# Kernel tuning notes

Measured on AMD Instinct MI355X. Metric: run time of the kernel, lower is better.

Reference implementation:

```python
import jax, jax.numpy as jnp
import numpy as np

NUM_HEADS = 16


def setup_inputs() -> dict:
    key = jax.random.key(0)
    ks = jax.random.split(key, 6)
    dim = 1024
    B, N = 4, 4096
    s = 1.0 / np.sqrt(dim)
    return {
        "x": jax.random.normal(ks[0], (B, N, dim), dtype=jnp.float32),
        "Wq": jax.random.normal(ks[1], (dim, dim), dtype=jnp.float32) * s,
        "Wk": jax.random.normal(ks[2], (dim, dim), dtype=jnp.float32) * s,
        "Wv": jax.random.normal(ks[3], (dim, dim), dtype=jnp.float32) * s,
        "Wo": jax.random.normal(ks[4], (dim, dim), dtype=jnp.float32) * s,
        "bo": jnp.zeros((dim,), dtype=jnp.float32),
    }


def reference(x, Wq, Wk, Wv, Wo, bo):
    # STAtten (linear attention) branch, no SNN, dropout = 0 (identity in eval).
    B, N, C = x.shape
    H = NUM_HEADS
    D = C // H
    scale = D ** (-0.5)

    def heads(W):
        # torch nn.Linear: y = x @ W.T ; then [B,N,H,D] -> [B,H,N,D]
        y = jnp.einsum('bnc,oc->bno', x, W)
        return y.reshape(B, N, H, D).transpose(0, 2, 1, 3)

    q = heads(Wq)
    k = heads(Wk)
    v = heads(Wv)

    kv = jnp.einsum('bhnd,bhne->bhde', k, v) * scale  # [B,H,D,D]
    out = jnp.einsum('bhnd,bhde->bhne', q, kv)        # [B,H,N,D]

    out = out.transpose(0, 2, 1, 3).reshape(B, N, C)
    return jnp.einsum('bnc,oc->bno', out, Wo) + bo
```

## Files before the change

### kernel.cpp

```cpp
#include <hip/hip_runtime.h>
#include <hip/hip_bf16.h>
#include <math.h>

typedef __hip_bfloat16 bf16;
typedef float f32x4 __attribute__((ext_vector_type(4)));
typedef short s16x8 __attribute__((ext_vector_type(8)));

typedef const __attribute__((address_space(1))) void* as1cvp;
typedef __attribute__((address_space(3))) void* as3vp;

__device__ __forceinline__ unsigned short f2bf(float f) {
  unsigned u = __float_as_uint(f);
  u += 0x7FFFu + ((u >> 16) & 1u);
  return (unsigned short)(u >> 16);
}
__device__ __forceinline__ float bf2f(unsigned short s) {
  return __uint_as_float(((unsigned)s) << 16);
}

__device__ __forceinline__ void gpu_barrier() {
  asm volatile("" ::: "memory");
  __builtin_amdgcn_s_barrier();
  asm volatile("" ::: "memory");
}

__device__ __forceinline__ void tri_decode(int xt, int* ti_out, int* tj_out) {
  int tj = (int)((sqrtf(8.0f * (float)xt + 1.0f) - 1.0f) * 0.5f);
  int tri = tj * (tj + 1) / 2;
  if (xt < tri) { --tj; tri = tj * (tj + 1) / 2; }
  else if (xt >= tri + tj + 1) { ++tj; tri = tj * (tj + 1) / 2; }
  *ti_out = xt - tri;
  *tj_out = tj;
}

__global__ __launch_bounds__(256) void cast_transpose(const float* __restrict__ x,
                                                      unsigned short* __restrict__ xb,
                                                      unsigned short* __restrict__ xT) {
  __shared__ unsigned short tl[128 * 136];
  const int n0 = blockIdx.x * 128, d0 = blockIdx.y * 128, b = blockIdx.z;
  const int t = threadIdx.x;

  const int rr0 = t >> 4;
  const int u   = t & 15;
  const int dd  = u * 8;
#pragma unroll
  for (int it = 0; it < 8; ++it) {
    const int rr = rr0 + it * 16;
    const float* src = x + ((long)(b * 4096 + n0 + rr)) * 1024 + d0 + dd;
    f32x4 v0 = *(const f32x4*)src;
    f32x4 v1 = *(const f32x4*)(src + 4);
    s16x8 o;
    o[0] = (short)f2bf(v0[0]); o[1] = (short)f2bf(v0[1]);
    o[2] = (short)f2bf(v0[2]); o[3] = (short)f2bf(v0[3]);
    o[4] = (short)f2bf(v1[0]); o[5] = (short)f2bf(v1[1]);
    o[6] = (short)f2bf(v1[2]); o[7] = (short)f2bf(v1[3]);
    *(s16x8*)&xb[((long)(b * 4096 + n0 + rr)) * 1024 + d0 + dd] = o;
    const int phys = u ^ (rr >> 3);
    *(s16x8*)&tl[rr * 136 + phys * 8] = o;
  }
  __syncthreads();

  const int nblk = t & 15, dblk = t >> 4;
  s16x8 row[8];
#pragma unroll
  for (int j = 0; j < 8; ++j) {
    const int n = nblk * 8 + j;
    const int phys = dblk ^ nblk;
    row[j] = *(const s16x8*)&tl[n * 136 + phys * 8];
  }
#pragma unroll
  for (int c = 0; c < 8; ++c) {
    s16x8 col;
#pragma unroll
    for (int j = 0; j < 8; ++j) col[j] = row[j][c];
    *(s16x8*)&xT[((long)(b * 1024 + d0 + dblk * 8 + c)) * 4096 + n0 + nblk * 8] = col;
  }
}

__global__ __launch_bounds__(256) void cast_weights(const float* __restrict__ Wq,
                                                    const float* __restrict__ Wk,
                                                    const float* __restrict__ Wv,
                                                    const float* __restrict__ Wo,
                                                    unsigned short* __restrict__ Wkb,
                                                    unsigned short* __restrict__ WvD,
                                                    unsigned short* __restrict__ Wqb,
                                                    unsigned short* __restrict__ Wob) {
  const int i = blockIdx.x * 256 + threadIdx.x;
  const int seg = blockIdx.y;
  const long flat = (long)i * 8;
  const float* src = (seg == 0) ? Wk : (seg == 1) ? Wv : (seg == 2) ? Wq : Wo;
  f32x4 v0 = *(const f32x4*)&src[flat];
  f32x4 v1 = *(const f32x4*)&src[flat + 4];
  s16x8 o;
  o[0] = (short)f2bf(v0[0]); o[1] = (short)f2bf(v0[1]);
  o[2] = (short)f2bf(v0[2]); o[3] = (short)f2bf(v0[3]);
  o[4] = (short)f2bf(v1[0]); o[5] = (short)f2bf(v1[1]);
  o[6] = (short)f2bf(v1[2]); o[7] = (short)f2bf(v1[3]);
  if (seg == 1) {
    const int r = (int)(flat >> 10), c = (int)(flat & 1023);
    *(s16x8*)&WvD[(long)r * 2048 + c] = o;
    *(s16x8*)&WvD[(long)r * 2048 + c + 1024] = o;
  } else {
    unsigned short* dst = (seg == 0) ? Wkb : (seg == 2) ? Wqb : Wob;
    *(s16x8*)&dst[flat] = o;
  }
}

template<bool OUTF32>
__global__ __launch_bounds__(512, 2) void gemm256(
    const bf16* __restrict__ A, int lda, long aOffY, long aOffZ,
    const bf16* __restrict__ Bt, int ldb, long btOffY, long btOffZ,
    void* __restrict__ Cv, int ldc, long cOffY, long cOffZ,
    const float* __restrict__ bias, int K, int NtN, int gridmode)
{
  __shared__ char lds[131072];

  const int Nx = gridDim.x, Ny = gridDim.y;
  const int lin = blockIdx.x + Nx * (blockIdx.y + Ny * blockIdx.z);
  const int tot = Nx * Ny * gridDim.z;
  const int swz = (lin & 7) * (tot >> 3) + (lin >> 3);
  const int xt = swz % Nx;
  const int r2 = swz / Nx;
  const int y = r2 % Ny, z = r2 / Ny;
  int ti, tj;
  if (gridmode == 1) {
    ti = (int)((0x3221110000ULL >> (4 * xt)) & 15);
    tj = (int)((0x3323213210ULL >> (4 * xt)) & 15);
  } else { ti = xt / NtN; tj = xt % NtN; }
  const int bm = ti * 256, bn = tj * 256;

  A  += (long)z * aOffZ + (long)y * aOffY;
  Bt += (long)z * btOffZ + (long)y * btOffY;

  const int tid  = threadIdx.x;
  const int wid  = tid >> 6;
  const int lane = tid & 63;
  const int wm = wid >> 2;
  const int wn = wid & 3;
  const int frow = lane & 15;
  const int fkb  = (lane >> 4) << 4;
  const unsigned xorv = (unsigned)((lane & 7) << 4);

  const int q0 = (tid * 16) ^ (((tid >> 3) & 7) << 4);
  const int q1 = (8192 + tid * 16) ^ (((tid >> 3) & 7) << 4);
  const int srow0 = q0 >> 7, scol0 = (q0 & 127) >> 1;
  const int srow1 = q1 >> 7, scol1 = (q1 & 127) >> 1;
  const bf16* ag0 = A  + (long)(bm + srow0) * lda + scol0;
  const bf16* ag1 = A  + (long)(bm + srow1) * lda + scol1;
  const bf16* bg0 = Bt + (long)(bn + srow0) * ldb + scol0;
  const bf16* bg1 = Bt + (long)(bn + srow1) * ldb + scol1;

#define STAGE_A(buf, half, kk) do {                                                  \
    __builtin_amdgcn_global_load_lds((as1cvp)(ag0 + (long)(half)*128*lda + (kk)),    \
        (as3vp)(lds + (buf)*32768 + (half)*16384 + wid*1024), 16, 0, 0);             \
    __builtin_amdgcn_global_load_lds((as1cvp)(ag1 + (long)(half)*128*lda + (kk)),    \
        (as3vp)(lds + (buf)*32768 + (half)*16384 + 8192 + wid*1024), 16, 0, 0);      \
  } while (0)
#define STAGE_B(buf, half, kk) do {                                                  \
    __builtin_amdgcn_global_load_lds((as1cvp)(bg0 + (long)(half)*128*ldb + (kk)),    \
        (as3vp)(lds + 65536 + (buf)*32768 + (half)*16384 + wid*1024), 16, 0, 0);     \
    __builtin_amdgcn_global_load_lds((as1cvp)(bg1 + (long)(half)*128*ldb + (kk)),    \
        (as3vp)(lds + 65536 + (buf)*32768 + (half)*16384 + 8192 + wid*1024), 16, 0, 0); \
  } while (0)

  const unsigned paBase = (unsigned)((wm * 64 + frow) * 128 + fkb);
  const unsigned pbBase = (unsigned)(((wn & 1) * 64 + frow) * 128 + fkb);
  const unsigned bHalf  = (unsigned)((wn >> 1) * 16384);

#define RD_A(dst, cur, Mh, mi, kh)                                                   \
  dst = *(const s16x8*)(lds + (cur)*32768 + (Mh)*16384 +                             \
                        ((paBase + (mi)*2048u + (kh)*64u) ^ xorv))
#define RD_B(dst, cur, nj, kh)                                                       \
  dst = *(const s16x8*)(lds + 65536 + (cur)*32768 + bHalf +                          \
                        ((pbBase + (nj)*2048u + (kh)*64u) ^ xorv))

#define MFMA16(base, bb)                                                             \
  __builtin_amdgcn_s_setprio(1);                                                     \
  _Pragma("unroll")                                                                  \
  for (int mi = 0; mi < 4; ++mi)                                                     \
    _Pragma("unroll")                                                                \
    for (int nj = 0; nj < 4; ++nj)                                                   \
      acc[(base) + mi][nj] = __builtin_amdgcn_mfma_f32_16x16x32_bf16(                \
          a[mi], bb[nj], acc[(base) + mi][nj], 0, 0, 0);                             \
  __builtin_amdgcn_s_setprio(0);

#define LGKM0 asm volatile("s_waitcnt lgkmcnt(0)" ::: "memory")
#define VM8   asm volatile("s_waitcnt vmcnt(8)" ::: "memory")

  f32x4 acc[8][4] = {};
  s16x8 a[4], b0[4], b1[4];
  const int NT = K >> 6;

  STAGE_A(0, 0, 0); STAGE_B(0, 0, 0); STAGE_B(0, 1, 0);
  STAGE_A(0, 1, 0);
  {
    const int kk = (NT > 1) ? 64 : 0;
    STAGE_A(1, 0, kk); STAGE_B(1, 0, kk); STAGE_B(1, 1, kk);
  }
  VM8;
  gpu_barrier();

  for (int t = 0; t < NT; ++t) {
    const int cur = t & 1, nxt = cur ^ 1;
    const int k1 = ((t + 1 < NT) ? (t + 1) : 0) * 64;
    const int k2 = ((t + 2 < NT) ? (t + 2) : 0) * 64;

#pragma unroll
    for (int mi = 0; mi < 4; ++mi) RD_A(a[mi], cur, 0, mi, 0);
#pragma unroll
    for (int nj = 0; nj < 4; ++nj) RD_B(b0[nj], cur, nj, 0);
    STAGE_A(nxt, 1, k1);
    gpu_barrier(); LGKM0;
    MFMA16(0, b0)
    gpu_barrier();

#pragma unroll
    for (int mi = 0; mi < 4; ++mi) RD_A(a[mi], cur, 0, mi, 1);
#pragma unroll
    for (int nj = 0; nj < 4; ++nj) RD_B(b1[nj], cur, nj, 1);
    gpu_barrier(); LGKM0;
    MFMA16(0, b1)
    VM8;
    gpu_barrier();

#pragma unroll
    for (int mi = 0; mi < 4; ++mi) RD_A(a[mi], cur, 1, mi, 0);
    STAGE_A(cur, 0, k2); STAGE_B(cur, 0, k2); STAGE_B(cur, 1, k2);
    gpu_barrier(); LGKM0;
    MFMA16(4, b0)
    gpu_barrier();

#pragma unroll
    for (int mi = 0; mi < 4; ++mi) RD_A(a[mi], cur, 1, mi, 1);
    gpu_barrier(); LGKM0;
    MFMA16(4, b1)
    VM8;
    gpu_barrier();
  }

  asm volatile("s_waitcnt vmcnt(0)" ::: "memory");

  const int crow0 = bm + wm * 64 + (lane >> 4) * 4;
  const int ccol0 = bn + wn * 64 + (lane & 15);
  if (OUTF32) {
    float* C = (float*)Cv + (long)z * cOffZ + (long)y * cOffY;
    float bs[4];
#pragma unroll
    for (int j = 0; j < 4; ++j) bs[j] = bias ? bias[ccol0 + j * 16] : 0.0f;
#pragma unroll
    for (int i = 0; i < 8; ++i) {
      const int row = crow0 + (i >> 2) * 128 + (i & 3) * 16;
#pragma unroll
      for (int j = 0; j < 4; ++j) {
        const int col = ccol0 + j * 16;
#pragma unroll
        for (int r = 0; r < 4; ++r)
          C[(long)(row + r) * ldc + col] = acc[i][j][r] + bs[j];
      }
    }
  } else {
    unsigned short* C = (unsigned short*)Cv + (long)z * cOffZ + (long)y * cOffY;
#pragma unroll
    for (int i = 0; i < 8; ++i) {
      const int row = crow0 + (i >> 2) * 128 + (i & 3) * 16;
#pragma unroll
      for (int j = 0; j < 4; ++j) {
        const int col = ccol0 + j * 16;
#pragma unroll
        for (int r = 0; r < 4; ++r)
          C[(long)(row + r) * ldc + col] = f2bf(acc[i][j][r]);
      }
    }
  }
#undef STAGE_A
#undef STAGE_B
#undef RD_A
#undef RD_B
#undef MFMA16
#undef LGKM0
#undef VM8
}

template<int MODE>
__global__ __launch_bounds__(256) void gemm128(
    const bf16* __restrict__ A0, const bf16* __restrict__ B0,
    void* __restrict__ Cv, const float* __restrict__ bias)
{
  __shared__ char lds[65536];

  const int Nx = gridDim.x;
  const int lin = blockIdx.x + Nx * blockIdx.y;
  const int tot = Nx * gridDim.y;
  const int swz = (lin & 7) * (tot >> 3) + (lin >> 3);
  const int xt = swz % Nx, yy = swz / Nx;

  const int lda = (MODE == 0) ? 4096 : 1024;
  const int ldb = lda;
  const int K   = 1024;
  int bm, bn;
  const bf16 *A, *Bt;
  if (MODE == 0) {
    int ti, tj; tri_decode(xt, &ti, &tj);
    bm = ti * 128; bn = tj * 128;
    const int z = yy >> 2, ys = yy & 3;
    A  = A0 + (long)z * 4194304 + ys * 1024;
    Bt = A;
  } else {
    bm = (xt >> 3) * 128; bn = (xt & 7) * 128;
    A  = A0;
    Bt = B0 + (long)yy * 1048576L;
  }

  const int tid  = threadIdx.x;
  const int wid  = tid >> 6;
  const int lane = tid & 63;
  const int wr = (wid >> 1) * 64, wc = (wid & 1) * 64;
  const int frow = lane & 15;
  const int fkb  = (lane >> 4) << 4;
  const unsigned xorv = (unsigned)((lane & 7) << 4);

  const int q0 = (tid * 16) ^ (((tid >> 3) & 7) << 4);
  const int srow0 = q0 >> 7, scol0 = (q0 & 127) >> 1;
  const bf16* ag = A  + (long)(bm + srow0) * lda + scol0;
  const bf16* bg = Bt + (long)(bn + srow0) * ldb + scol0;

#define STG128(buf, kk) do {                                                         \
    _Pragma("unroll")                                                                \
    for (int i = 0; i < 4; ++i) {                                                    \
      __builtin_amdgcn_global_load_lds((as1cvp)(ag + (long)i * 32 * lda + (kk)),     \
          (as3vp)(lds + (buf) * 16384 + i * 4096 + tid * 16), 16, 0, 0);             \
      __builtin_amdgcn_global_load_lds((as1cvp)(bg + (long)i * 32 * ldb + (kk)),     \
          (as3vp)(lds + 32768 + (buf) * 16384 + i * 4096 + tid * 16), 16, 0, 0);     \
    }                                                                                \
  } while (0)

  const unsigned paB = (unsigned)((wr + frow) * 128 + fkb);
  const unsigned pbB = (unsigned)((wc + frow) * 128 + fkb);

  f32x4 acc[4][4] = {};
  const int NT = K >> 6;

  STG128(0, 0);
  asm volatile("s_waitcnt vmcnt(0)" ::: "memory");
  gpu_barrier();

  for (int t = 0; t < NT; ++t) {
    const int cur = t & 1;
    if (t + 1 < NT) STG128(cur ^ 1, (t + 1) * 64);
    s16x8 a[4][2], b[4][2];
#pragma unroll
    for (int mi = 0; mi < 4; ++mi)
#pragma unroll
      for (int kh = 0; kh < 2; ++kh)
        a[mi][kh] = *(const s16x8*)(lds + cur * 16384 +
                                    ((paB + mi * 2048u + kh * 64u) ^ xorv));
#pragma unroll
    for (int nj = 0; nj < 4; ++nj)
#pragma unroll
      for (int kh = 0; kh < 2; ++kh)
        b[nj][kh] = *(const s16x8*)(lds + 32768 + cur * 16384 +
                                    ((pbB + nj * 2048u + kh * 64u) ^ xorv));
    asm volatile("s_waitcnt lgkmcnt(0)" ::: "memory");
#pragma unroll
    for (int mi = 0; mi < 4; ++mi)
#pragma unroll
      for (int nj = 0; nj < 4; ++nj) {
        acc[mi][nj] = __builtin_amdgcn_mfma_f32_16x16x32_bf16(a[mi][0], b[nj][0], acc[mi][nj], 0, 0, 0);
        acc[mi][nj] = __builtin_amdgcn_mfma_f32_16x16x32_bf16(a[mi][1], b[nj][1], acc[mi][nj], 0, 0, 0);
      }
    asm volatile("s_waitcnt vmcnt(0)" ::: "memory");
    gpu_barrier();
  }

  const int r0 = wr + (lane >> 4) * 4;
  const int c0t = wc + (lane & 15);
  if (MODE == 0) {
    float* C = (float*)Cv + (long)(yy * 36 + xt) * 16384;
#pragma unroll
    for (int mi = 0; mi < 4; ++mi)
#pragma unroll
      for (int nj = 0; nj < 4; ++nj)
#pragma unroll
        for (int r = 0; r < 4; ++r)
          C[(r0 + mi * 16 + r) * 128 + c0t + nj * 16] = acc[mi][nj][r];
  } else if (MODE == 2) {
    unsigned short* C = (unsigned short*)Cv + (long)yy * 2097152;
#pragma unroll
    for (int mi = 0; mi < 4; ++mi)
#pragma unroll
      for (int nj = 0; nj < 4; ++nj)
#pragma unroll
        for (int r = 0; r < 4; ++r) {
          const float v = acc[mi][nj][r];
          const unsigned short h = f2bf(v);
          const long idx = (long)(bm + r0 + mi * 16 + r) * 2048 + bn + c0t + nj * 16;
          C[idx] = h;
          C[idx + 1024] = f2bf(v - bf2f(h));
        }
  } else {
    unsigned short* C = (unsigned short*)Cv + (long)yy * 1048576;
#pragma unroll
    for (int mi = 0; mi < 4; ++mi)
#pragma unroll
      for (int nj = 0; nj < 4; ++nj)
#pragma unroll
        for (int r = 0; r < 4; ++r)
          C[(long)(bm + r0 + mi * 16 + r) * 1024 + bn + c0t + nj * 16] =
              f2bf(acc[mi][nj][r]);
  }
#undef STG128
}

__global__ __launch_bounds__(256) void gred128(const float* __restrict__ Gp,
                                               unsigned short* __restrict__ Gb) {
  const int tile = blockIdx.x >> 2, sub = blockIdx.x & 3;
  const int z = blockIdx.y;
  int ti, tj; tri_decode(tile, &ti, &tj);
  const int t = threadIdx.x;
  const int rr = sub * 32 + (t >> 3);
  const int c0 = (t & 7) * 16;

  f32x4 s[4] = {};
#pragma unroll
  for (int y = 0; y < 4; ++y) {
    const float* p = Gp + ((long)(z * 4 + y) * 36 + tile) * 16384 + rr * 128 + c0;
#pragma unroll
    for (int q = 0; q < 4; ++q) {
      f32x4 v = *(const f32x4*)&p[q * 4];
#pragma unroll
      for (int j = 0; j < 4; ++j) s[q][j] += v[j];
    }
  }
  unsigned short hi[16];
#pragma unroll
  for (int q = 0; q < 4; ++q)
#pragma unroll
    for (int j = 0; j < 4; ++j) hi[q * 4 + j] = f2bf(s[q][j]);
  unsigned short* base = Gb + (long)z * 1048576;
  const int R0 = ti * 128 + rr, C0 = tj * 128 + c0;
#pragma unroll
  for (int q = 0; q < 2; ++q)
    *(s16x8*)&base[(long)R0 * 1024 + C0 + q * 8] = *(const s16x8*)&hi[q * 8];
  if (ti != tj) {
#pragma unroll
    for (int j = 0; j < 16; ++j)
      base[(long)(C0 + j) * 1024 + R0] = hi[j];
  }
}

template<int OUTMODE>
__global__ __launch_bounds__(256) void gemm64(
    const bf16* __restrict__ A, int lda, long aOffZ,
    const bf16* __restrict__ Bt, int ldb, long btOffZ,
    void* __restrict__ Cv, int ldc, long cOffZ, int loOff,
    int K, int NtN, int diag, int ksplit)
{
  __shared__ char lds[32768];

  const int Nx = gridDim.x;
  const int lin = blockIdx.x + Nx * blockIdx.y;
  const int tot = Nx * gridDim.y;
  const int swz = (lin & 7) * (tot >> 3) + (lin >> 3);
  const int xt = swz % Nx, y = swz / Nx;
  const int zb = y / ksplit, zs = y % ksplit;
  const int ti = diag ? xt : xt / NtN;
  const int tj = diag ? xt : xt % NtN;
  const int bm = ti * 64, bn = tj * 64;

  A  += (long)zb * aOffZ + (long)zs * K;
  Bt += (long)zb * btOffZ + (long)zs * K;

  const int tid  = threadIdx.x;
  const int wid  = tid >> 6;
  const int lane = tid & 63;
  const int wr = (wid >> 1) * 32, wc = (wid & 1) * 32;
  const int frow = lane & 15;
  const int fkb  = (lane >> 4) << 4;
  const unsigned xorv = (unsigned)((lane & 7) << 4);

  const int q0 = (tid * 16) ^ (((tid >> 3) & 7) << 4);
  const int q1 = (4096 + tid * 16) ^ (((tid >> 3) & 7) << 4);
  const int srow0 = q0 >> 7, scol0 = (q0 & 127) >> 1;
  const int srow1 = q1 >> 7, scol1 = (q1 & 127) >> 1;
  const bf16* ag0 = A  + (long)(bm + srow0) * lda + scol0;
  const bf16* ag1 = A  + (long)(bm + srow1) * lda + scol1;
  const bf16* bg0 = Bt + (long)(bn + srow0) * ldb + scol0;
  const bf16* bg1 = Bt + (long)(bn + srow1) * ldb + scol1;

#define STAGE64(buf, kk) do {                                                        \
    __builtin_amdgcn_global_load_lds((as1cvp)(ag0 + (kk)),                           \
        (as3vp)(lds + (buf)*8192 + wid*1024), 16, 0, 0);                             \
    __builtin_amdgcn_global_load_lds((as1cvp)(ag1 + (kk)),                           \
        (as3vp)(lds + (buf)*8192 + 4096 + wid*1024), 16, 0, 0);                      \
    __builtin_amdgcn_global_load_lds((as1cvp)(bg0 + (kk)),                           \
        (as3vp)(lds + 16384 + (buf)*8192 + wid*1024), 16, 0, 0);                     \
    __builtin_amdgcn_global_load_lds((as1cvp)(bg1 + (kk)),                           \
        (as3vp)(lds + 16384 + (buf)*8192 + 4096 + wid*1024), 16, 0, 0);              \
  } while (0)

  const unsigned paB = (unsigned)((wr + frow) * 128 + fkb);
  const unsigned pbB = (unsigned)((wc + frow) * 128 + fkb);

  f32x4 acc[2][2] = {};
  const int NT = K >> 6;

  STAGE64(0, 0);
  asm volatile("s_waitcnt vmcnt(0)" ::: "memory");
  gpu_barrier();

  for (int t = 0; t < NT; ++t) {
    const int cur = t & 1;
    if (t + 1 < NT) STAGE64(cur ^ 1, (t + 1) * 64);
    s16x8 a[2][2], b[2][2];
#pragma unroll
    for (int mi = 0; mi < 2; ++mi)
#pragma unroll
      for (int kh = 0; kh < 2; ++kh)
        a[mi][kh] = *(const s16x8*)(lds + cur * 8192 +
                                    ((paB + mi * 2048u + kh * 64u) ^ xorv));
#pragma unroll
    for (int nj = 0; nj < 2; ++nj)
#pragma unroll
      for (int kh = 0; kh < 2; ++kh)
        b[nj][kh] = *(const s16x8*)(lds + 16384 + cur * 8192 +
                                    ((pbB + nj * 2048u + kh * 64u) ^ xorv));
    asm volatile("s_waitcnt lgkmcnt(0)" ::: "memory");
#pragma unroll
    for (int mi = 0; mi < 2; ++mi)
#pragma unroll
      for (int nj = 0; nj < 2; ++nj) {
        acc[mi][nj] = __builtin_amdgcn_mfma_f32_16x16x32_bf16(a[mi][0], b[nj][0], acc[mi][nj], 0, 0, 0);
        acc[mi][nj] = __builtin_amdgcn_mfma_f32_16x16x32_bf16(a[mi][1], b[nj][1], acc[mi][nj], 0, 0, 0);
      }
    asm volatile("s_waitcnt vmcnt(0)" ::: "memory");
    gpu_barrier();
  }

  const int r0 = wr + (lane >> 4) * 4;
  const int c0 = wc + (lane & 15);
  if (OUTMODE == 1) {
    float* C = (float*)Cv + (long)y * cOffZ + (long)xt * 4096;
#pragma unroll
    for (int mi = 0; mi < 2; ++mi)
#pragma unroll
      for (int nj = 0; nj < 2; ++nj)
#pragma unroll
        for (int r = 0; r < 4; ++r)
          C[(r0 + mi * 16 + r) * 64 + c0 + nj * 16] = acc[mi][nj][r];
  } else {
    unsigned short* C = (unsigned short*)Cv + (long)y * cOffZ;
#pragma unroll
    for (int mi = 0; mi < 2; ++mi)
#pragma unroll
      for (int nj = 0; nj < 2; ++nj)
#pragma unroll
        for (int r = 0; r < 4; ++r) {
          const float v = acc[mi][nj][r];
          const unsigned short h = f2bf(v);
          const long idx = (long)(bm + r0 + mi * 16 + r) * ldc + bn + c0 + nj * 16;
          C[idx] = h;
          if (OUTMODE == 2) C[idx + loOff] = f2bf(v - bf2f(h));
        }
  }
#undef STAGE64
}

__global__ __launch_bounds__(256) void yt_kernel(const float* __restrict__ Up,
                                                 const unsigned short* __restrict__ Wqb,
                                                 unsigned short* __restrict__ Yt) {
  __shared__ float Ul[64 * 64];
  __shared__ float Wql[64 * 68];
  const int cblk = blockIdx.x, h = blockIdx.y, z = blockIdx.z;
  const int t = threadIdx.x;

  {
    const int d = t >> 2, e0 = (t & 3) * 16;
#pragma unroll
    for (int q = 0; q < 4; ++q) {
      f32x4 s = {};
#pragma unroll
      for (int sp = 0; sp < 4; ++sp) {
        f32x4 v = *(const f32x4*)&Up[((long)(z * 4 + sp) * 16 + h) * 4096 + d * 64 + e0 + q * 4];
#pragma unroll
        for (int j = 0; j < 4; ++j) s[j] += v[j];
      }
      *(f32x4*)&Ul[d * 64 + e0 + q * 4] = s;
    }
    const unsigned short* wp = Wqb + (long)(h * 64 + d) * 1024 + cblk * 64 + e0;
#pragma unroll
    for (int q = 0; q < 2; ++q) {
      s16x8 w = *(const s16x8*)&wp[q * 8];
#pragma unroll
      for (int j = 0; j < 8; ++j) Wql[d * 68 + e0 + q * 8 + j] = bf2f((unsigned short)w[j]);
    }
  }
  __syncthreads();

  const int jc = t >> 2, e0 = (t & 3) * 16;
  f32x4 acc[4] = {};
  for (int d = 0; d < 64; ++d) {
    const float w = Wql[d * 68 + jc];
    const float* ur = &Ul[d * 64 + e0];
#pragma unroll
    for (int q = 0; q < 4; ++q) {
      f32x4 u4 = *(const f32x4*)&ur[q * 4];
#pragma unroll
      for (int j = 0; j < 4; ++j) acc[q][j] += w * u4[j];
    }
  }
  unsigned short* yp = Yt + (long)z * 1048576 + (long)(cblk * 64 + jc) * 1024 + h * 64 + e0;
#pragma unroll
  for (int q = 0; q < 4; ++q)
#pragma unroll
    for (int j = 0; j < 4; ++j) yp[q * 4 + j] = f2bf(acc[q][j] * 0.125f);
}

extern "C" void kernel_launch(void* const* d_in, const int* in_sizes, int n_in,
                              void* d_out, int out_size, void* d_ws, size_t ws_size,
                              hipStream_t stream) {
  const float* x  = (const float*)d_in[0];
  const float* Wq = (const float*)d_in[1];
  const float* Wk = (const float*)d_in[2];
  const float* Wv = (const float*)d_in[3];
  const float* Wo = (const float*)d_in[4];
  const float* bo = (const float*)d_in[5];
  float* out = (float*)d_out;

  char* ws = (char*)d_ws;
  unsigned short* xb  = (unsigned short*)(ws);
  unsigned short* xT  = (unsigned short*)(ws + 33554432);
  unsigned short* Gb  = (unsigned short*)(ws + 33554432);
  unsigned short* Wkb = (unsigned short*)(ws + 67108864);
  unsigned short* WvD = (unsigned short*)(ws + 71303168);
  unsigned short* Wqb = (unsigned short*)(ws + 75497472);
  unsigned short* Wob = (unsigned short*)(ws + 77594624);
  float*          Gp  = (float*)         (ws + 79691776);
  unsigned short* Thl = (unsigned short*)(ws + 79691776);
  float*          Up  = (float*)         (ws + 96468992);
  unsigned short* Yt  = (unsigned short*)(ws + 113246208);
  unsigned short* R   = (unsigned short*)(ws + 121634816);

  cast_transpose<<<dim3(32, 8, 4), 256, 0, stream>>>(x, xb, xT);
  cast_weights<<<dim3(512, 4), 256, 0, stream>>>(Wq, Wk, Wv, Wo, Wkb, WvD, Wqb, Wob);

  gemm128<0><<<dim3(36, 16), 256, 0, stream>>>(
      (const bf16*)xT, nullptr, (void*)Gp, nullptr);

  gred128<<<dim3(144, 4), 256, 0, stream>>>(Gp, Gb);

  gemm128<2><<<dim3(64, 4), 256, 0, stream>>>(
      (const bf16*)Wkb, (const bf16*)Gb, (void*)Thl, nullptr);

  gemm64<1><<<dim3(16, 16), 256, 0, stream>>>(
      (const bf16*)Thl, 2048, 2097152L, (const bf16*)WvD, 2048, 0L,
      (void*)Up, 64, 65536L, 0, 512, 1, 1, 4);

  yt_kernel<<<dim3(16, 16, 4), 256, 0, stream>>>(Up, Wqb, Yt);

  gemm128<3><<<dim3(64, 4), 256, 0, stream>>>(
      (const bf16*)Wob, (const bf16*)Yt, (void*)R, nullptr);

  gemm256<true><<<dim3(64, 1, 4), 512, 0, stream>>>(
      (const bf16*)xb, 1024, 0L, 4194304L,
      (const bf16*)R, 1024, 0L, 1048576L,
      (void*)out, 1024, 0L, 4194304L,
      bo, 1024, 4, 0);
}
```

Measured before the change: 178.9 us.

## Drop hi/lo bf16 split and store Gram partials as bf16

The Gram-matrix partial tiles are now written as bf16 instead of fp32, which halves the traffic for the write and for the reduction read. The hi/lo compensated split of the Wk·G product and the duplicated Wv operand are removed, so the following GEMM runs with half the K (256 instead of 512) and half the operand bytes. The cost is lower precision: partial sums are rounded to bf16 before the reduction, and the error-compensation term is gone, which may push numerical error toward tolerance limits.

```diff
diff --git a/kernel.cpp b/kernel.cpp
--- a/kernel.cpp
+++ b/kernel.cpp
@@ -82,7 +82,7 @@
                                                     const float* __restrict__ Wv,
                                                     const float* __restrict__ Wo,
                                                     unsigned short* __restrict__ Wkb,
-                                                    unsigned short* __restrict__ WvD,
+                                                    unsigned short* __restrict__ Wvb,
                                                     unsigned short* __restrict__ Wqb,
                                                     unsigned short* __restrict__ Wob) {
   const int i = blockIdx.x * 256 + threadIdx.x;
@@ -96,14 +96,8 @@
   o[2] = (short)f2bf(v0[2]); o[3] = (short)f2bf(v0[3]);
   o[4] = (short)f2bf(v1[0]); o[5] = (short)f2bf(v1[1]);
   o[6] = (short)f2bf(v1[2]); o[7] = (short)f2bf(v1[3]);
-  if (seg == 1) {
-    const int r = (int)(flat >> 10), c = (int)(flat & 1023);
-    *(s16x8*)&WvD[(long)r * 2048 + c] = o;
-    *(s16x8*)&WvD[(long)r * 2048 + c + 1024] = o;
-  } else {
-    unsigned short* dst = (seg == 0) ? Wkb : (seg == 2) ? Wqb : Wob;
-    *(s16x8*)&dst[flat] = o;
-  }
+  unsigned short* dst = (seg == 0) ? Wkb : (seg == 1) ? Wvb : (seg == 2) ? Wqb : Wob;
+  *(s16x8*)&dst[flat] = o;
 }
 
 template<bool OUTF32>
@@ -375,28 +369,14 @@
   const int r0 = wr + (lane >> 4) * 4;
   const int c0t = wc + (lane & 15);
   if (MODE == 0) {
-    float* C = (float*)Cv + (long)(yy * 36 + xt) * 16384;
+    unsigned short* C = (unsigned short*)Cv + (long)(yy * 36 + xt) * 16384;
 #pragma unroll
     for (int mi = 0; mi < 4; ++mi)
 #pragma unroll
       for (int nj = 0; nj < 4; ++nj)
 #pragma unroll
         for (int r = 0; r < 4; ++r)
-          C[(r0 + mi * 16 + r) * 128 + c0t + nj * 16] = acc[mi][nj][r];
-  } else if (MODE == 2) {
-    unsigned short* C = (unsigned short*)Cv + (long)yy * 2097152;
-#pragma unroll
-    for (int mi = 0; mi < 4; ++mi)
-#pragma unroll
-      for (int nj = 0; nj < 4; ++nj)
-#pragma unroll
-        for (int r = 0; r < 4; ++r) {
-          const float v = acc[mi][nj][r];
-          const unsigned short h = f2bf(v);
-          const long idx = (long)(bm + r0 + mi * 16 + r) * 2048 + bn + c0t + nj * 16;
-          C[idx] = h;
-          C[idx + 1024] = f2bf(v - bf2f(h));
-        }
+          C[(r0 + mi * 16 + r) * 128 + c0t + nj * 16] = f2bf(acc[mi][nj][r]);
   } else {
     unsigned short* C = (unsigned short*)Cv + (long)yy * 1048576;
 #pragma unroll
@@ -411,7 +391,7 @@
 #undef STG128
 }
 
-__global__ __launch_bounds__(256) void gred128(const float* __restrict__ Gp,
+__global__ __launch_bounds__(256) void gred128(const unsigned short* __restrict__ Gp,
                                                unsigned short* __restrict__ Gb) {
   const int tile = blockIdx.x >> 2, sub = blockIdx.x & 3;
   const int z = blockIdx.y;
@@ -420,22 +400,20 @@
   const int rr = sub * 32 + (t >> 3);
   const int c0 = (t & 7) * 16;
 
-  f32x4 s[4] = {};
+  float s[16] = {};
 #pragma unroll
   for (int y = 0; y < 4; ++y) {
-    const float* p = Gp + ((long)(z * 4 + y) * 36 + tile) * 16384 + rr * 128 + c0;
-#pragma unroll
-    for (int q = 0; q < 4; ++q) {
-      f32x4 v = *(const f32x4*)&p[q * 4];
-#pragma unroll
-      for (int j = 0; j < 4; ++j) s[q][j] += v[j];
+    const unsigned short* p = Gp + ((long)(z * 4 + y) * 36 + tile) * 16384 + rr * 128 + c0;
+#pragma unroll
+    for (int q = 0; q < 2; ++q) {
+      s16x8 v = *(const s16x8*)&p[q * 8];
+#pragma unroll
+      for (int j = 0; j < 8; ++j) s[q * 8 + j] += bf2f((unsigned short)v[j]);
     }
   }
   unsigned short hi[16];
 #pragma unroll
-  for (int q = 0; q < 4; ++q)
-#pragma unroll
-    for (int j = 0; j < 4; ++j) hi[q * 4 + j] = f2bf(s[q][j]);
+  for (int j = 0; j < 16; ++j) hi[j] = f2bf(s[j]);
   unsigned short* base = Gb + (long)z * 1048576;
   const int R0 = ti * 128 + rr, C0 = tj * 128 + c0;
 #pragma unroll
@@ -631,29 +609,29 @@
   unsigned short* xT  = (unsigned short*)(ws + 33554432);
   unsigned short* Gb  = (unsigned short*)(ws + 33554432);
   unsigned short* Wkb = (unsigned short*)(ws + 67108864);
-  unsigned short* WvD = (unsigned short*)(ws + 71303168);
+  unsigned short* Wvb = (unsigned short*)(ws + 71303168);
   unsigned short* Wqb = (unsigned short*)(ws + 75497472);
   unsigned short* Wob = (unsigned short*)(ws + 77594624);
-  float*          Gp  = (float*)         (ws + 79691776);
-  unsigned short* Thl = (unsigned short*)(ws + 79691776);
+  unsigned short* Gp  = (unsigned short*)(ws + 79691776);
+  unsigned short* T   = (unsigned short*)(ws + 79691776);
   float*          Up  = (float*)         (ws + 96468992);
   unsigned short* Yt  = (unsigned short*)(ws + 113246208);
   unsigned short* R   = (unsigned short*)(ws + 121634816);
 
   cast_transpose<<<dim3(32, 8, 4), 256, 0, stream>>>(x, xb, xT);
-  cast_weights<<<dim3(512, 4), 256, 0, stream>>>(Wq, Wk, Wv, Wo, Wkb, WvD, Wqb, Wob);
+  cast_weights<<<dim3(512, 4), 256, 0, stream>>>(Wq, Wk, Wv, Wo, Wkb, Wvb, Wqb, Wob);
 
   gemm128<0><<<dim3(36, 16), 256, 0, stream>>>(
       (const bf16*)xT, nullptr, (void*)Gp, nullptr);
 
   gred128<<<dim3(144, 4), 256, 0, stream>>>(Gp, Gb);
 
-  gemm128<2><<<dim3(64, 4), 256, 0, stream>>>(
-      (const bf16*)Wkb, (const bf16*)Gb, (void*)Thl, nullptr);
+  gemm128<3><<<dim3(64, 4), 256, 0, stream>>>(
+      (const bf16*)Wkb, (const bf16*)Gb, (void*)T, nullptr);
 
   gemm64<1><<<dim3(16, 16), 256, 0, stream>>>(
-      (const bf16*)Thl, 2048, 2097152L, (const bf16*)WvD, 2048, 0L,
-      (void*)Up, 64, 65536L, 0, 512, 1, 1, 4);
+      (const bf16*)T, 1024, 1048576L, (const bf16*)Wvb, 1024, 0L,
+      (void*)Up, 64, 65536L, 0, 256, 1, 1, 4);
 
   yt_kernel<<<dim3(16, 16, 4), 256, 0, stream>>>(Up, Wqb, Yt);
 
```

Result: faster. 170.3 us (-4.8%).
